# Performance work log

Hardware: AMD Instinct MI355X
Metric: run time of the kernel (lower is better)

## Reference

```python
import jax, jax.numpy as jnp
import numpy as np

TOP_K = 8
NUM_EXPERTS = 64
TEMPERATURE = 1.0
ALPHA = 0.01
EPS = 1e-20


def setup_inputs() -> dict:
    key = jax.random.key(0)
    k1, k2 = jax.random.split(key)
    hidden_states = jax.random.normal(k1, (4, 8192, 1024), dtype=jnp.float32)
    # kaiming_uniform-ish scale for the router weight
    bound = 1.0 / np.sqrt(1024.0)
    weight = jax.random.uniform(k2, (NUM_EXPERTS, 1024), dtype=jnp.float32,
                                minval=-bound, maxval=bound)
    return {"hidden_states": hidden_states, "weight": weight}


def reference(hidden_states, weight):
    bsz, seq_len, hidden_dim = hidden_states.shape
    flat = hidden_states.reshape(-1, hidden_dim)            # [N, H], N = bsz*seq_len
    logits = jnp.einsum('nh,eh->ne', flat, weight) / TEMPERATURE  # [N, E]
    scores = jax.nn.softmax(logits, axis=-1)                # [N, E]
    topk_weight, topk_idx = jax.lax.top_k(scores, TOP_K)    # [N, k] each
    # renormalize top-k probabilities
    topk_weight = topk_weight / (topk_weight.sum(axis=-1, keepdims=True) + EPS)
    # aux load-balancing loss (seq_aux=False branch), scores detached
    scores_aux = jax.lax.stop_gradient(scores)
    idx_flat = topk_idx.reshape(-1)                         # [N*k]
    ce = jnp.zeros((NUM_EXPERTS,), dtype=jnp.float32).at[idx_flat].add(1.0)
    ce = ce / idx_flat.shape[0]                             # mean of one-hot rows
    pi = scores_aux.mean(axis=0)                            # [E]
    fi = ce * NUM_EXPERTS
    aux_loss = (pi * fi).sum() * ALPHA
    return topk_idx, topk_weight, aux_loss
```

## Files before the change

### kernel.cpp

```cpp
#include <hip/hip_runtime.h>

#define H 1024
#define E 64
#define BT 64
#define THETA 4e-4f

typedef __attribute__((ext_vector_type(4))) float f4;
typedef __attribute__((ext_vector_type(16))) float f32x16;
typedef __bf16 bf16x8 __attribute__((ext_vector_type(8)));
typedef unsigned int u32;
typedef __attribute__((ext_vector_type(4))) u32 u32x4;

__device__ __forceinline__ u32 cvtpk_bf16(float a, float b) {
    u32 r;
    asm("v_cvt_pk_bf16_f32 %0, %1, %2" : "=v"(r) : "v"(a), "v"(b));
    return r;
}
__device__ __forceinline__ float asfloat(u32 u) { union { u32 u; float f; } c; c.u = u; return c.f; }

__device__ __forceinline__ void split8(f4 a, f4 b, u32x4& hi, u32x4& lo) {
    float x0[4] = {a.x, a.z, b.x, b.z};
    float x1[4] = {a.y, a.w, b.y, b.w};
    #pragma unroll
    for (int i = 0; i < 4; ++i) {
        u32 h = cvtpk_bf16(x0[i], x1[i]);
        float r0 = x0[i] - asfloat(h << 16);
        float r1 = x1[i] - asfloat(h & 0xFFFF0000u);
        hi[i] = h;
        lo[i] = cvtpk_bf16(r0, r1);
    }
}

__global__ __launch_bounds__(256, 2)
void gate_main(const float* __restrict__ hs, const float* __restrict__ wt,
               float* __restrict__ out, float* __restrict__ pi_ws,
               float* __restrict__ ce_ws, unsigned int* __restrict__ risk_cnt,
               unsigned int* __restrict__ risk_list, unsigned int risk_cap,
               int n_tokens) {
    __shared__ float smem[16384];
    const int t = threadIdx.x;
    const int wave = t >> 6, lane = t & 63;
    const int tok_base = blockIdx.x * BT;

    const int srow = t >> 3;
    const int sjp  = t & 7;
    const int ssw  = ((sjp ^ (srow & 7)) << 4);

    const int lr   = lane & 31;
    const int kh   = lane >> 5;
    const int wrow = (wave >> 1) * 32;
    const int wcol = (wave & 1) * 32;
    const int aOff = (wrow + lr) * 128;
    const int bOff = 16384 + (wcol + lr) * 128;
    const int rsw  = lr & 7;

    f32x16 acc0, acc1;
    #pragma unroll
    for (int i = 0; i < 16; ++i) { acc0[i] = 0.f; acc1[i] = 0.f; }

    f4 sreg[8];
    char* sb = (char*)smem;

    auto stage_load = [&](int c) {
        const float* ph = hs + (size_t)(tok_base + srow) * H + c * 64 + sjp * 8;
        sreg[0] = *(const f4*)ph;
        sreg[1] = *(const f4*)(ph + 4);
        sreg[2] = *(const f4*)(ph + 32 * H);
        sreg[3] = *(const f4*)(ph + 32 * H + 4);
        const float* pw = wt + (size_t)srow * H + c * 64 + sjp * 8;
        sreg[4] = *(const f4*)pw;
        sreg[5] = *(const f4*)(pw + 4);
        sreg[6] = *(const f4*)(pw + 32 * H);
        sreg[7] = *(const f4*)(pw + 32 * H + 4);
    };
    auto stage_write = [&](int c) {
        char* bb = sb + (c & 1) * 32768;
        u32x4 hi, lo;
        split8(sreg[0], sreg[1], hi, lo);
        *(u32x4*)(bb + srow * 128 + ssw) = hi;
        *(u32x4*)(bb + 8192 + srow * 128 + ssw) = lo;
        split8(sreg[2], sreg[3], hi, lo);
        *(u32x4*)(bb + (srow + 32) * 128 + ssw) = hi;
        *(u32x4*)(bb + 8192 + (srow + 32) * 128 + ssw) = lo;
        split8(sreg[4], sreg[5], hi, lo);
        *(u32x4*)(bb + 16384 + srow * 128 + ssw) = hi;
        *(u32x4*)(bb + 24576 + srow * 128 + ssw) = lo;
        split8(sreg[6], sreg[7], hi, lo);
        *(u32x4*)(bb + 16384 + (srow + 32) * 128 + ssw) = hi;
        *(u32x4*)(bb + 24576 + (srow + 32) * 128 + ssw) = lo;
    };

    stage_load(0);
    stage_write(0);
    #pragma unroll 2
    for (int c = 0; c < 16; ++c) {
        __syncthreads();
        if (c < 15) stage_load(c + 1);
        const char* cb = sb + (c & 1) * 32768;
        #pragma unroll
        for (int kk = 0; kk < 4; ++kk) {
            const int g = ((kk * 2 + kh) ^ rsw) << 4;
            bf16x8 ah = *(const bf16x8*)(cb + aOff + g);
            bf16x8 al = *(const bf16x8*)(cb + 8192 + aOff + g);
            bf16x8 bh = *(const bf16x8*)(cb + bOff + g);
            bf16x8 bl = *(const bf16x8*)(cb + 8192 + bOff + g);
            acc0 = __builtin_amdgcn_mfma_f32_32x32x16_bf16(ah, bh, acc0, 0, 0, 0);
            acc1 = __builtin_amdgcn_mfma_f32_32x32x16_bf16(ah, bl, acc1, 0, 0, 0);
            acc1 = __builtin_amdgcn_mfma_f32_32x32x16_bf16(al, bh, acc1, 0, 0, 0);
        }
        __builtin_amdgcn_sched_barrier(0);
        if (c < 15) stage_write(c + 1);
    }
    __syncthreads();

    float* S = smem;
    f4* S4 = (f4*)smem;
    float* recip = smem + 4352;
    float* hist  = smem + 4416;
    float* pi3   = smem + 4480;
    {
        const int col = wcol + lr;
        #pragma unroll
        for (int gq = 0; gq < 4; ++gq)
            #pragma unroll
            for (int q = 0; q < 4; ++q) {
                const int row = wrow + gq * 8 + kh * 4 + q;
                S[row * 68 + col] = acc0[gq * 4 + q] + acc1[gq * 4 + q];
            }
    }
    if (t < 64) hist[t] = 0.f;
    __syncthreads();

    {
        const int tok = t >> 2, q = t & 3;
        f4 v[4];
        #pragma unroll
        for (int c2 = 0; c2 < 4; ++c2) v[c2] = S4[tok * 17 + q * 4 + c2];
        float m = v[0].x;
        #pragma unroll
        for (int c2 = 0; c2 < 4; ++c2)
            m = fmaxf(m, fmaxf(fmaxf(v[c2].x, v[c2].y), fmaxf(v[c2].z, v[c2].w)));
        m = fmaxf(m, __shfl_xor(m, 1, 64));
        m = fmaxf(m, __shfl_xor(m, 2, 64));
        float lsum = 0.f;
        #pragma unroll
        for (int c2 = 0; c2 < 4; ++c2) {
            v[c2].x = __expf(v[c2].x - m); v[c2].y = __expf(v[c2].y - m);
            v[c2].z = __expf(v[c2].z - m); v[c2].w = __expf(v[c2].w - m);
            lsum += (v[c2].x + v[c2].y) + (v[c2].z + v[c2].w);
        }
        #pragma unroll
        for (int c2 = 0; c2 < 4; ++c2) S4[tok * 17 + q * 4 + c2] = v[c2];
        lsum += __shfl_xor(lsum, 1, 64);
        lsum += __shfl_xor(lsum, 2, 64);
        if (q == 0) recip[tok] = 1.0f / lsum;
    }
    __syncthreads();

    const int selw = blockIdx.x & 3;
    if (wave == selw) {
        const int tok = lane;
        const int tok_g = tok_base + tok;
        float val[9]; int idx[9];
        #pragma unroll
        for (int r = 0; r < 9; ++r) { val[r] = -1.f; idx[r] = 0; }
        #pragma unroll
        for (int c2 = 0; c2 < 16; ++c2) {
            f4 v = S4[tok * 17 + c2];
            float e4[4] = {v.x, v.y, v.z, v.w};
            #pragma unroll
            for (int u = 0; u < 4; ++u) {
                float cv = e4[u]; int ci = c2 * 4 + u;
                #pragma unroll
                for (int r = 0; r < 9; ++r) {
                    const bool g = cv > val[r];
                    const float tv = val[r]; const int ti = idx[r];
                    val[r] = g ? cv : tv;  idx[r] = g ? ci : ti;
                    cv = g ? tv : cv;      ci = g ? ti : ci;
                }
            }
        }
        const float s8 = ((val[0] + val[1]) + (val[2] + val[3]))
                       + ((val[4] + val[5]) + (val[6] + val[7]));
        const float wsum = s8 + 1e-20f;
        f4* out4 = (f4*)out;
        f4 o;
        o.x = (float)idx[0]; o.y = (float)idx[1]; o.z = (float)idx[2]; o.w = (float)idx[3];
        out4[(size_t)tok_g * 2] = o;
        o.x = (float)idx[4]; o.y = (float)idx[5]; o.z = (float)idx[6]; o.w = (float)idx[7];
        out4[(size_t)tok_g * 2 + 1] = o;
        const size_t wb = (size_t)n_tokens * 2;
        o.x = val[0] / wsum; o.y = val[1] / wsum; o.z = val[2] / wsum; o.w = val[3] / wsum;
        out4[wb + (size_t)tok_g * 2] = o;
        o.x = val[4] / wsum; o.y = val[5] / wsum; o.z = val[6] / wsum; o.w = val[7] / wsum;
        out4[wb + (size_t)tok_g * 2 + 1] = o;
        #pragma unroll
        for (int r = 0; r < 8; ++r) atomicAdd(&hist[idx[r]], 1.0f);
        float ming = 1e30f;
        #pragma unroll
        for (int r = 0; r < 8; ++r)
            ming = fminf(ming, (val[r] - val[r + 1]) / fmaxf(val[r], 1e-30f));
        if (ming < THETA) {
            unsigned int pos = atomicAdd(risk_cnt, 1u);
            if (pos < risk_cap) risk_list[pos] = (unsigned int)tok_g;
        }
    } else {
        const int third = ((wave - selw) & 3) - 1;
        const int e = lane;
        const int t0 = third * 21;
        const int t1 = (third == 2) ? 64 : (t0 + 21);
        float part = 0.f;
        for (int tok = t0; tok < t1; ++tok)
            part = fmaf(S[tok * 68 + e], recip[tok], part);
        pi3[third * 64 + e] = part;
    }
    __syncthreads();
    if (t < 64)       atomicAdd(&pi_ws[t], pi3[t] + pi3[64 + t] + pi3[128 + t]);
    else if (t < 128) atomicAdd(&ce_ws[t - 64], hist[t - 64]);
}

__global__ __launch_bounds__(256)
void gate_fixup(const float* __restrict__ hs, const float* __restrict__ wt,
                float* __restrict__ out, const unsigned int* __restrict__ risk_cnt,
                const unsigned int* __restrict__ risk_list, unsigned int risk_cap,
                int n_tokens, const float* __restrict__ pi_ws,
                const float* __restrict__ ce_ws) {
    __shared__ float hrow[H];
    __shared__ double red[256];
    const int t = threadIdx.x;

    if (blockIdx.x == 0 && t < 64) {
        double pi = (double)pi_ws[t] / (double)n_tokens;
        double ce = (double)ce_ws[t] / ((double)n_tokens * 8.0);
        double term = pi * ce * 64.0;
        #pragma unroll
        for (int off = 32; off > 0; off >>= 1) term += __shfl_xor(term, off, 64);
        if (t == 0) out[(size_t)n_tokens * 16] = (float)(term * 0.01);
    }

    unsigned int cnt = *risk_cnt;
    if (cnt > risk_cap) cnt = risk_cap;

    for (unsigned int u = blockIdx.x; u < cnt; u += gridDim.x) {
        const int tok = (int)risk_list[u];
        ((float4*)hrow)[t] = ((const float4*)(hs + (size_t)tok * H))[t];
        __syncthreads();

        const int e = t >> 2, sl = t & 3;
        const float4* wp = (const float4*)wt + (size_t)e * 256;
        const float4* hp = (const float4*)hrow;
        double acc = 0.0;
        #pragma unroll 8
        for (int k4 = 0; k4 < 64; ++k4) {
            float4 wv = wp[k4 * 4 + sl];
            float4 hv = hp[k4 * 4 + sl];
            acc = fma((double)wv.x, (double)hv.x, acc);
            acc = fma((double)wv.y, (double)hv.y, acc);
            acc = fma((double)wv.z, (double)hv.z, acc);
            acc = fma((double)wv.w, (double)hv.w, acc);
        }
        red[t] = acc;
        __syncthreads();

        if (t < 64) {
            const int lane = t;
            double lg = red[t * 4] + red[t * 4 + 1] + red[t * 4 + 2] + red[t * 4 + 3];
            double m = lg;
            #pragma unroll
            for (int off = 32; off > 0; off >>= 1) {
                double o = __shfl_xor(m, off, 64);
                m = (o > m) ? o : m;
            }
            const double p = exp(lg - m);
            double v = lg, psum = 0.0, mypv = 0.0;
            int myidx = 0;
            for (int r = 0; r < 8; ++r) {
                double bv = v; int bi = lane;
                #pragma unroll
                for (int off = 32; off > 0; off >>= 1) {
                    double ov = __shfl_xor(bv, off, 64);
                    int    oi = __shfl_xor(bi, off, 64);
                    if (ov > bv || (ov == bv && oi < bi)) { bv = ov; bi = oi; }
                }
                double pw = __shfl(p, bi, 64);
                psum += pw;
                if (lane == r) { myidx = bi; mypv = pw; }
                if (lane == bi) v = -1e300;
            }
            const double wsum = psum + 1e-20;
            if (lane < 8) {
                out[(size_t)tok * 8 + lane] = (float)myidx;
                out[(size_t)n_tokens * 8 + (size_t)tok * 8 + lane] = (float)(mypv / wsum);
            }
        }
        __syncthreads();
    }
}

extern "C" void kernel_launch(void* const* d_in, const int* in_sizes, int n_in,
                              void* d_out, int out_size, void* d_ws, size_t ws_size,
                              hipStream_t stream) {
    const float* hs = (const float*)d_in[0];
    const float* wt = (const float*)d_in[1];
    float* out = (float*)d_out;
    const int n_tokens = in_sizes[0] / H;

    float* pi_ws = (float*)d_ws;
    float* ce_ws = (float*)((char*)d_ws + 256);
    unsigned int* risk_cnt  = (unsigned int*)((char*)d_ws + 512);
    unsigned int* risk_list = (unsigned int*)((char*)d_ws + 1024);
    unsigned int risk_cap = (unsigned int)((ws_size > 1024 ? (ws_size - 1024) : 0) / 4);
    if (risk_cap > (unsigned int)n_tokens) risk_cap = (unsigned int)n_tokens;

    size_t zbytes = ws_size < 1024 ? ws_size : 1024;
    hipMemsetAsync(d_ws, 0, zbytes, stream);

    gate_main<<<n_tokens / BT, 256, 0, stream>>>(hs, wt, out, pi_ws, ce_ws,
                                                 risk_cnt, risk_list, risk_cap, n_tokens);
    gate_fixup<<<256, 256, 0, stream>>>(hs, wt, out, risk_cnt, risk_list, risk_cap,
                                        n_tokens, pi_ws, ce_ws);
}
```

Baseline: 274.7 us.

## Stage fp32 tiles via async global-to-LDS loads and split K across eight waves

Replaces the register-staged load, bf16 split and LDS write with direct global_load_lds copies of raw fp32 tiles into swizzled LDS. The hi/lo bf16 split now happens after reading from LDS. Blocks grow to 512 threads, with the two wave halves each taking half the K range and reducing partial accumulators through shared memory. The aim is to drop VGPR staging and add overlap and occupancy, at the cost of redoing the split per wave, an extra reduction step, and the 64 KB LDS footprint limiting resident blocks. The risk threshold for the exact fixup pass is also halved, which means fewer tokens get recomputed.

```diff
diff --git a/kernel.cpp b/kernel.cpp
--- a/kernel.cpp
+++ b/kernel.cpp
@@ -3,7 +3,7 @@
 #define H 1024
 #define E 64
 #define BT 64
-#define THETA 4e-4f
+#define THETA 2e-4f
 
 typedef __attribute__((ext_vector_type(4))) float f4;
 typedef __attribute__((ext_vector_type(16))) float f32x16;
@@ -31,7 +31,14 @@
     }
 }
 
-__global__ __launch_bounds__(256, 2)
+__device__ __forceinline__ void async16(const void* g, void* l) {
+    __builtin_amdgcn_global_load_lds(
+        (const __attribute__((address_space(1))) unsigned int*)g,
+        (__attribute__((address_space(3))) unsigned int*)l,
+        16, 0, 0);
+}
+
+__global__ __launch_bounds__(512, 4)
 void gate_main(const float* __restrict__ hs, const float* __restrict__ wt,
                float* __restrict__ out, float* __restrict__ pi_ws,
                float* __restrict__ ce_ws, unsigned int* __restrict__ risk_cnt,
@@ -42,96 +49,101 @@
     const int wave = t >> 6, lane = t & 63;
     const int tok_base = blockIdx.x * BT;
 
-    const int srow = t >> 3;
-    const int sjp  = t & 7;
-    const int ssw  = ((sjp ^ (srow & 7)) << 4);
-
-    const int lr   = lane & 31;
-    const int kh   = lane >> 5;
-    const int wrow = (wave >> 1) * 32;
-    const int wcol = (wave & 1) * 32;
-    const int aOff = (wrow + lr) * 128;
-    const int bOff = 16384 + (wcol + lr) * 128;
-    const int rsw  = lr & 7;
+    const int lr  = lane & 31;
+    const int kh  = lane >> 5;
+    const int q4  = wave & 3;
+    const int kh2 = wave >> 2;
+    const int wrow = (q4 >> 1) * 32;
+    const int wcol = (q4 & 1) * 32;
 
     f32x16 acc0, acc1;
     #pragma unroll
     for (int i = 0; i < 16; ++i) { acc0[i] = 0.f; acc1[i] = 0.f; }
 
-    f4 sreg[8];
     char* sb = (char*)smem;
 
-    auto stage_load = [&](int c) {
-        const float* ph = hs + (size_t)(tok_base + srow) * H + c * 64 + sjp * 8;
-        sreg[0] = *(const f4*)ph;
-        sreg[1] = *(const f4*)(ph + 4);
-        sreg[2] = *(const f4*)(ph + 32 * H);
-        sreg[3] = *(const f4*)(ph + 32 * H + 4);
-        const float* pw = wt + (size_t)srow * H + c * 64 + sjp * 8;
-        sreg[4] = *(const f4*)pw;
-        sreg[5] = *(const f4*)(pw + 4);
-        sreg[6] = *(const f4*)(pw + 32 * H);
-        sreg[7] = *(const f4*)(pw + 32 * H + 4);
+    auto stage = [&](int c, int b) {
+        char* bb = sb + b * 32768;
+        #pragma unroll
+        for (int q = 0; q < 4; ++q) {
+            const int L = q * 512 + t;
+            const int r = (L >> 4) & 63;
+            const int j = L & 15;
+            const int srcj = j ^ (r & 7);
+            const float* src = (q < 2)
+                ? hs + (size_t)(tok_base + r) * H + c * 64 + srcj * 4
+                : wt + (size_t)r * H + c * 64 + srcj * 4;
+            async16(src, bb + ((q * 512 + wave * 64) << 4));
+        }
     };
-    auto stage_write = [&](int c) {
-        char* bb = sb + (c & 1) * 32768;
-        u32x4 hi, lo;
-        split8(sreg[0], sreg[1], hi, lo);
-        *(u32x4*)(bb + srow * 128 + ssw) = hi;
-        *(u32x4*)(bb + 8192 + srow * 128 + ssw) = lo;
-        split8(sreg[2], sreg[3], hi, lo);
-        *(u32x4*)(bb + (srow + 32) * 128 + ssw) = hi;
-        *(u32x4*)(bb + 8192 + (srow + 32) * 128 + ssw) = lo;
-        split8(sreg[4], sreg[5], hi, lo);
-        *(u32x4*)(bb + 16384 + srow * 128 + ssw) = hi;
-        *(u32x4*)(bb + 24576 + srow * 128 + ssw) = lo;
-        split8(sreg[6], sreg[7], hi, lo);
-        *(u32x4*)(bb + 16384 + (srow + 32) * 128 + ssw) = hi;
-        *(u32x4*)(bb + 24576 + (srow + 32) * 128 + ssw) = lo;
-    };
-
-    stage_load(0);
-    stage_write(0);
+
+    stage(0, 0);
+    const int arow = wrow + lr;
+    const int brow = wcol + lr;
+    const int abase = arow * 256;
+    const int bbase = 16384 + brow * 256;
+    const int asw = arow & 7, bsw = brow & 7;
+
     #pragma unroll 2
     for (int c = 0; c < 16; ++c) {
         __syncthreads();
-        if (c < 15) stage_load(c + 1);
+        if (c < 15) stage(c + 1, (c + 1) & 1);
         const char* cb = sb + (c & 1) * 32768;
         #pragma unroll
-        for (int kk = 0; kk < 4; ++kk) {
-            const int g = ((kk * 2 + kh) ^ rsw) << 4;
-            bf16x8 ah = *(const bf16x8*)(cb + aOff + g);
-            bf16x8 al = *(const bf16x8*)(cb + 8192 + aOff + g);
-            bf16x8 bh = *(const bf16x8*)(cb + bOff + g);
-            bf16x8 bl = *(const bf16x8*)(cb + 8192 + bOff + g);
+        for (int ks = 0; ks < 2; ++ks) {
+            const int s = kh2 * 8 + ks * 4 + kh * 2;
+            f4 a0 = *(const f4*)(cb + abase + ((s ^ asw) << 4));
+            f4 a1 = *(const f4*)(cb + abase + (((s + 1) ^ asw) << 4));
+            f4 b0 = *(const f4*)(cb + bbase + ((s ^ bsw) << 4));
+            f4 b1 = *(const f4*)(cb + bbase + (((s + 1) ^ bsw) << 4));
+            u32x4 ahp, alp, bhp, blp;
+            split8(a0, a1, ahp, alp);
+            split8(b0, b1, bhp, blp);
+            const bf16x8 ah = __builtin_bit_cast(bf16x8, ahp);
+            const bf16x8 al = __builtin_bit_cast(bf16x8, alp);
+            const bf16x8 bh = __builtin_bit_cast(bf16x8, bhp);
+            const bf16x8 bl = __builtin_bit_cast(bf16x8, blp);
             acc0 = __builtin_amdgcn_mfma_f32_32x32x16_bf16(ah, bh, acc0, 0, 0, 0);
             acc1 = __builtin_amdgcn_mfma_f32_32x32x16_bf16(ah, bl, acc1, 0, 0, 0);
             acc1 = __builtin_amdgcn_mfma_f32_32x32x16_bf16(al, bh, acc1, 0, 0, 0);
         }
-        __builtin_amdgcn_sched_barrier(0);
-        if (c < 15) stage_write(c + 1);
     }
     __syncthreads();
 
     float* S = smem;
     f4* S4 = (f4*)smem;
-    float* recip = smem + 4352;
-    float* hist  = smem + 4416;
-    float* pi3   = smem + 4480;
+    float* P2    = smem + 4352;
+    float* recip = smem + 8448;
+    float* hist  = smem + 8512;
+    float* pi7   = smem + 8576;
+
     {
-        const int col = wcol + lr;
-        #pragma unroll
-        for (int gq = 0; gq < 4; ++gq)
+        float vs[16];
+        #pragma unroll
+        for (int i = 0; i < 16; ++i) vs[i] = acc0[i] + acc1[i];
+        if (kh2) {
             #pragma unroll
-            for (int q = 0; q < 4; ++q) {
-                const int row = wrow + gq * 8 + kh * 4 + q;
-                S[row * 68 + col] = acc0[gq * 4 + q] + acc1[gq * 4 + q];
-            }
-    }
-    if (t < 64) hist[t] = 0.f;
+            for (int gq = 0; gq < 4; ++gq)
+                #pragma unroll
+                for (int qq = 0; qq < 4; ++qq)
+                    P2[q4 * 1024 + (qq + gq * 8 + kh * 4) * 32 + lr] = vs[gq * 4 + qq];
+        }
+        if (t < 64) hist[t] = 0.f;
+        __syncthreads();
+        if (!kh2) {
+            #pragma unroll
+            for (int gq = 0; gq < 4; ++gq)
+                #pragma unroll
+                for (int qq = 0; qq < 4; ++qq) {
+                    const int row = qq + gq * 8 + kh * 4;
+                    S[(wrow + row) * 68 + wcol + lr] =
+                        vs[gq * 4 + qq] + P2[q4 * 1024 + row * 32 + lr];
+                }
+        }
+    }
     __syncthreads();
 
-    {
+    if (t < 256) {
         const int tok = t >> 2, q = t & 3;
         f4 v[4];
         #pragma unroll
@@ -157,7 +169,7 @@
     }
     __syncthreads();
 
-    const int selw = blockIdx.x & 3;
+    const int selw = blockIdx.x & 7;
     if (wave == selw) {
         const int tok = lane;
         const int tok_g = tok_base + tok;
@@ -205,18 +217,23 @@
             if (pos < risk_cap) risk_list[pos] = (unsigned int)tok_g;
         }
     } else {
-        const int third = ((wave - selw) & 3) - 1;
+        const int sev = ((wave - selw) & 7) - 1;
         const int e = lane;
-        const int t0 = third * 21;
-        const int t1 = (third == 2) ? 64 : (t0 + 21);
+        const int t0 = sev * 9;
+        const int t1 = (sev == 6) ? 64 : (t0 + 9);
         float part = 0.f;
         for (int tok = t0; tok < t1; ++tok)
             part = fmaf(S[tok * 68 + e], recip[tok], part);
-        pi3[third * 64 + e] = part;
+        pi7[sev * 64 + e] = part;
     }
     __syncthreads();
-    if (t < 64)       atomicAdd(&pi_ws[t], pi3[t] + pi3[64 + t] + pi3[128 + t]);
-    else if (t < 128) atomicAdd(&ce_ws[t - 64], hist[t - 64]);
+    if (t < 64) {
+        const float p = ((pi7[t] + pi7[64 + t]) + (pi7[128 + t] + pi7[192 + t]))
+                      + ((pi7[256 + t] + pi7[320 + t]) + pi7[384 + t]);
+        atomicAdd(&pi_ws[t], p);
+    } else if (t < 128) {
+        atomicAdd(&ce_ws[t - 64], hist[t - 64]);
+    }
 }
 
 __global__ __launch_bounds__(256)
@@ -315,7 +332,7 @@
     size_t zbytes = ws_size < 1024 ? ws_size : 1024;
     hipMemsetAsync(d_ws, 0, zbytes, stream);
 
-    gate_main<<<n_tokens / BT, 256, 0, stream>>>(hs, wt, out, pi_ws, ce_ws,
+    gate_main<<<n_tokens / BT, 512, 0, stream>>>(hs, wt, out, pi_ws, ce_ws,
                                                  risk_cnt, risk_list, risk_cap, n_tokens);
     gate_fixup<<<256, 256, 0, stream>>>(hs, wt, out, risk_cnt, risk_list, risk_cap,
                                         n_tokens, pi_ws, ce_ws);
```

Result: faster. 251.4 us (-8.5%).
